# Performance work log

Hardware: AMD Instinct MI355X
Metric: run time of the kernel (lower is better)

The kernel has to match this reference:

```python
import jax, jax.numpy as jnp
import numpy as np

N_NODES = 20000
N_EDGES = 80000
D = 128       # in_dim_node == in_dim_edge == hidden dims
ITERS = 15    # mp_iterations
EPS = 1e-5    # torch LayerNorm default eps


def _mlp(h, W0, b0, W1, b1, W2, b2, gamma, beta):
    """Linear-ReLU-Linear-ReLU-Linear-LayerNorm (hidden_layers=2)."""
    h = jax.nn.relu(h @ W0 + b0)
    h = jax.nn.relu(h @ W1 + b1)
    h = h @ W2 + b2
    mu = jnp.mean(h, axis=-1, keepdims=True)
    var = jnp.var(h, axis=-1, keepdims=True)
    return gamma * (h - mu) * jax.lax.rsqrt(var + EPS) + beta


def setup_inputs() -> dict:
    key = jax.random.key(0)
    ks = iter(jax.random.split(key, 32))

    def lin(fi, fo):
        bnd = 1.0 / np.sqrt(fi)
        W = jax.random.uniform(next(ks), (ITERS, fi, fo), minval=-bnd, maxval=bnd, dtype=jnp.float32)
        b = jax.random.uniform(next(ks), (ITERS, fo), minval=-bnd, maxval=bnd, dtype=jnp.float32)
        return W, b

    x = jax.random.normal(next(ks), (N_NODES, D), dtype=jnp.float32)
    edge_attr = jax.random.normal(next(ks), (N_EDGES, D), dtype=jnp.float32)
    edge_index = jax.random.randint(next(ks), (2, N_EDGES), 0, N_NODES)

    eW0, eB0 = lin(3 * D, D)   # edge MLP input = cat(src, dest, edge) = 384
    eW1, eB1 = lin(D, D)
    eW2, eB2 = lin(D, D)
    nW0, nB0 = lin(2 * D, D)   # node MLP input = cat(x, agg) = 256
    nW1, nB1 = lin(D, D)
    nW2, nB2 = lin(D, D)
    ones = jnp.ones((ITERS, D), jnp.float32)
    zeros = jnp.zeros((ITERS, D), jnp.float32)

    return dict(x=x, edge_attr=edge_attr,
                eW0=eW0, eB0=eB0, eW1=eW1, eB1=eB1, eW2=eW2, eB2=eB2, eG=ones, eBeta=zeros,
                nW0=nW0, nB0=nB0, nW1=nW1, nB1=nB1, nW2=nW2, nB2=nB2, nG=ones, nBeta=zeros,
                edge_index=edge_index)


def reference(x, edge_attr, eW0, eB0, eW1, eB1, eW2, eB2, eG, eBeta,
              nW0, nB0, nW1, nB1, nW2, nB2, nG, nBeta, edge_index):
    row, col = edge_index[0], edge_index[1]
    n = x.shape[0]
    params = (eW0, eB0, eW1, eB1, eW2, eB2, eG, eBeta,
              nW0, nB0, nW1, nB1, nW2, nB2, nG, nBeta)

    def step(carry, p):
        xc, ec = carry
        (ew0, eb0, ew1, eb1, ew2, eb2, eg, ebt,
         nw0, nb0, nw1, nb1, nw2, nb2, ng, nbt) = p
        # EdgeProcessor: gather + MLP, then FullResidualConnection (add previous)
        e_in = jnp.concatenate([xc[row], xc[col], ec], axis=-1)        # [E, 3D]
        ec = _mlp(e_in, ew0, eb0, ew1, eb1, ew2, eb2, eg, ebt) + ec
        # NodeProcessor: scatter_sum over destination nodes + MLP + residual
        agg = jax.ops.segment_sum(ec, col, num_segments=n)             # [N, D]
        n_in = jnp.concatenate([xc, agg], axis=-1)                     # [N, 2D]
        xc = _mlp(n_in, nw0, nb0, nw1, nb1, nw2, nb2, ng, nbt) + xc
        return (xc, ec), None

    (x, edge_attr), _ = jax.lax.scan(step, (x, edge_attr), params)
    return x, edge_attr
```

## Files before the change

kernel.cpp:

```cpp
#include <hip/hip_runtime.h>
#include <hip/hip_bf16.h>

typedef __hip_bfloat16 bf16;
typedef __attribute__((ext_vector_type(8))) short short8;
typedef __attribute__((ext_vector_type(4))) float f32x4;

#define NN 20000
#define NE 80000
#define DD 128
#define NITER 15
#define HSTRIDE 136

__device__ inline void gload16(const void* g, void* l) {
  __builtin_amdgcn_global_load_lds(
      (const __attribute__((address_space(1))) void*)g,
      (__attribute__((address_space(3))) void*)l, 16, 0, 0);
}

__device__ inline void waitVm(int n) {
  switch (n) {
    case 0: asm volatile("s_waitcnt vmcnt(0)" ::: "memory"); break;
    case 1: asm volatile("s_waitcnt vmcnt(1)" ::: "memory"); break;
    case 2: asm volatile("s_waitcnt vmcnt(2)" ::: "memory"); break;
    case 3: asm volatile("s_waitcnt vmcnt(3)" ::: "memory"); break;
    default: asm volatile("s_waitcnt vmcnt(4)" ::: "memory"); break;
  }
}

__device__ inline float bfbits2f(unsigned int hi16) {
  union { unsigned int u; float f; } c; c.u = hi16; return c.f;
}

__device__ inline float readin(const void* p, int i, int fl) {
  return fl ? (float)((const bf16*)p)[i] : ((const float*)p)[i];
}

__global__ void detzero_kernel(const unsigned short* __restrict__ x,
                               int* __restrict__ counts, int* __restrict__ flag) {
  const int bid = blockIdx.x, t = threadIdx.x;
  if (bid < 79) {
    int i = bid * 256 + t;
    if (i < NN) counts[i] = 0;
    return;
  }
  __shared__ int cs[256], ct[256];
  int sane = 0, tot = 0;
  for (int i = 2 * t; i < 16384; i += 512) {
    unsigned short v = x[i];
    int e = (v >> 7) & 0xFF;
    tot++;
    if (v == 0 || (e >= 80 && e <= 170)) sane++;
  }
  cs[t] = sane; ct[t] = tot;
  __syncthreads();
  for (int o = 128; o > 0; o >>= 1) {
    if (t < o) { cs[t] += cs[t + o]; ct[t] += ct[t + o]; }
    __syncthreads();
  }
  if (t == 0) *flag = (cs[0] * 10 > ct[0] * 7) ? 1 : 0;
}

#define CX  (NN * DD)
#define CE  (NE * DD)
#define CW0 (NITER * 384 * DD)
#define CW1 (NITER * 128 * DD)
#define CNW0 (NITER * 256 * DD)
#define CB  (NITER * DD)
#define BX0 CX
#define BX1 (BX0 + CE)
#define BX7 (BX1 + CW0 + CW1 + CW1 + CNW0 + CW1 + CW1)
#define BX8 (BX7 + 10 * CB)

struct CvtP {
  const void *x, *e;
  const void* w[6];
  bf16 *xb, *eb;
  bf16* wt[6];
  const void* bs[10];
  float* bd[10];
  const int* flag;
};

__global__ void convert_all(CvtP P) {
  const int fl = *P.flag;
  const int gstride = gridDim.x * 256;
  for (int i = blockIdx.x * 256 + threadIdx.x; i < BX8; i += gstride) {
    if (i < BX0) {
      P.xb[i] = (bf16)readin(P.x, i, fl);
    } else if (i < BX1) {
      P.eb[i - BX0] = (bf16)readin(P.e, i - BX0, fl);
    } else if (i < BX7) {
      int j = i - BX1, w;
      if (j < CW0) { w = 0; }
      else if ((j -= CW0) < CW1) { w = 1; }
      else if ((j -= CW1) < CW1) { w = 2; }
      else if ((j -= CW1) < CNW0) { w = 3; }
      else if ((j -= CNW0) < CW1) { w = 4; }
      else { j -= CW1; w = 5; }
      const int K = (w == 0) ? 384 : (w == 3) ? 256 : 128;
      float v = readin(P.w[w], j, fl);
      int it = j / (K * DD);
      int rem = j - it * K * DD;
      int k = rem >> 7, n = rem & 127;
      P.wt[w][(size_t)it * K * DD + (size_t)n * K + k] = (bf16)v;
    } else {
      int j = i - BX7;
      int b = j / CB, r = j - b * CB;
      P.bd[b][r] = readin(P.bs[b], r, fl);
    }
  }
}

template<int K0, int AMODE, int NW>
__global__ __launch_bounds__(NW * 64, NW == 8 ? 6 : 4) void fused_mlp(
    const bf16* S0b,
    const bf16* S1b,
    const int*  __restrict__ eidx,
    const bf16* __restrict__ W0t, const bf16* __restrict__ W1t,
    const bf16* __restrict__ W2t,
    const float* __restrict__ b0, const float* __restrict__ b1,
    const float* __restrict__ b2,
    const float* __restrict__ gamma, const float* __restrict__ beta,
    bf16* st, int M)
{
  constexpr int NS1  = K0 / 32;
  constexpr int ROWS = NW * 16;
  constexpr int DN   = (NW == 8) ? 1 : 2;
  __shared__ __align__(16) bf16 Bls[2][128 * 32];
  __shared__ __align__(16) bf16 Hls[ROWS * HSTRIDE];

  const int tid  = threadIdx.x;
  const int lane = tid & 63;
  const int wv   = tid >> 6;
  const int l15  = lane & 15, quad = lane >> 4;
  const int m0   = blockIdx.x * ROWS;
  const int scol = tid >> 2;
  const int sk8  = (tid & 3) * 8;

  const int rowm = min(m0 + wv * 16 + l15, M - 1);
  int ir = 0, ic = 0;
  if (AMODE == 1) { ir = eidx[rowm]; ic = eidx[NE + rowm]; }

  auto dmaW = [&](const bf16* W, int K, int kk, int buf) {
    gload16(W + (size_t)scol * K + kk + sk8, &Bls[buf][scol * 32 + sk8]);
    if (NW == 4)
      gload16(W + (size_t)(scol + 64) * K + kk + sk8, &Bls[buf][(scol + 64) * 32 + sk8]);
  };
  auto gatherA = [&](int kk, short8* a) {
    const int ks = (kk & 127) + quad * 8;
    const bf16* base;
    if (AMODE == 1) {
      const int seg = kk >> 7;
      base = (seg == 0) ? S0b + (size_t)ir * DD
           : (seg == 1) ? S0b + (size_t)ic * DD
                        : S1b + (size_t)rowm * DD;
    } else {
      base = (kk >> 7) ? S1b + (size_t)rowm * DD
                       : S0b + (size_t)rowm * DD;
    }
    *a = *(const short8*)(base + ks);
  };

  f32x4 acc[8];
  auto zacc = [&]() {
#pragma unroll
    for (int j = 0; j < 8; j++) acc[j] = (f32x4){0.f, 0.f, 0.f, 0.f};
  };
  auto slabMfmaA = [&](short8 a, int buf) {
    short8 bfr[8];
#pragma unroll
    for (int ni = 0; ni < 8; ni++)
      bfr[ni] = *(const short8*)&Bls[buf][(ni * 16 + l15) * 32 + quad * 8];
#pragma unroll
    for (int ni = 0; ni < 8; ni++)
      acc[ni] = __builtin_amdgcn_mfma_f32_16x16x32_bf16(a, bfr[ni], acc[ni], 0, 0, 0);
  };
  auto slabMfmaH = [&](int kk, int buf) {
    short8 a = *(const short8*)&Hls[(wv * 16 + l15) * HSTRIDE + kk + quad * 8];
    short8 bfr[8];
#pragma unroll
    for (int ni = 0; ni < 8; ni++)
      bfr[ni] = *(const short8*)&Bls[buf][(ni * 16 + l15) * 32 + quad * 8];
#pragma unroll
    for (int ni = 0; ni < 8; ni++)
      acc[ni] = __builtin_amdgcn_mfma_f32_16x16x32_bf16(a, bfr[ni], acc[ni], 0, 0, 0);
  };
  auto writeH = [&](const float* bias) {
    float bv[8];
#pragma unroll
    for (int ni = 0; ni < 8; ni++) bv[ni] = bias[ni * 16 + l15];
#pragma unroll
    for (int r = 0; r < 4; r++) {
      const int row = wv * 16 + quad * 4 + r;
#pragma unroll
      for (int ni = 0; ni < 8; ni++)
        Hls[row * HSTRIDE + ni * 16 + l15] = (bf16)fmaxf(acc[ni][r] + bv[ni], 0.f);
    }
  };

  zacc();
  short8 aCur, aNxt;
  dmaW(W0t, K0, 0, 0);
  gatherA(0, &aCur);
#pragma unroll
  for (int s = 0; s < NS1; s++) {
    int cnt;
    if (s + 1 < NS1) {
      dmaW(W0t, K0, (s + 1) * 32, (s + 1) & 1);
      gatherA((s + 1) * 32, &aNxt);
      cnt = 1 + DN + 1;
    } else {
      dmaW(W1t, 128, 0, NS1 & 1);
      cnt = 1 + DN;
    }
    waitVm(cnt);
    __builtin_amdgcn_s_barrier();
    __builtin_amdgcn_sched_barrier(0);
    slabMfmaA(aCur, s & 1);
    __builtin_amdgcn_sched_barrier(0);
    __builtin_amdgcn_s_barrier();
    aCur = aNxt;
  }
  writeH(b0);

  zacc();
#pragma unroll
  for (int s = 0; s < 4; s++) {
    if (s < 3) dmaW(W1t, 128, (s + 1) * 32, (NS1 + s + 1) & 1);
    else       dmaW(W2t, 128, 0,            (NS1 + 4) & 1);
    waitVm(DN);
    __builtin_amdgcn_s_barrier();
    __builtin_amdgcn_sched_barrier(0);
    slabMfmaH(s * 32, (NS1 + s) & 1);
    __builtin_amdgcn_sched_barrier(0);
    __builtin_amdgcn_s_barrier();
  }
  writeH(b1);

  zacc();
#pragma unroll
  for (int s = 0; s < 4; s++) {
    int cnt = 0;
    if (s < 3) { dmaW(W2t, 128, (s + 1) * 32, (NS1 + 4 + s + 1) & 1); cnt = DN; }
    waitVm(cnt);
    __builtin_amdgcn_s_barrier();
    __builtin_amdgcn_sched_barrier(0);
    slabMfmaH(s * 32, (NS1 + 4 + s) & 1);
    if (s < 3) {
      __builtin_amdgcn_sched_barrier(0);
      __builtin_amdgcn_s_barrier();
    }
  }

  float bv[8], gv[8], btv[8];
#pragma unroll
  for (int ni = 0; ni < 8; ni++) {
    const int col = ni * 16 + l15;
    bv[ni] = b2[col]; gv[ni] = gamma[col]; btv[ni] = beta[col];
  }
#pragma unroll
  for (int r = 0; r < 4; r++) {
    float a = 0.f, bq = 0.f;
#pragma unroll
    for (int ni = 0; ni < 8; ni++) {
      const float v = acc[ni][r] + bv[ni];
      a += v; bq += v * v;
    }
#pragma unroll
    for (int off = 1; off < 16; off <<= 1) {
      a  += __shfl_xor(a, off);
      bq += __shfl_xor(bq, off);
    }
    const float mu = a * (1.0f / 128.0f);
    const float var = fmaxf(bq * (1.0f / 128.0f) - mu * mu, 0.0f);
    const float rs = rsqrtf(var + 1e-5f);
    const int m = m0 + wv * 16 + quad * 4 + r;
    if (m < M) {
#pragma unroll
      for (int ni = 0; ni < 8; ni++) {
        const int col = ni * 16 + l15;
        const float v = acc[ni][r] + bv[ni];
        const float lnv = (v - mu) * rs * gv[ni] + btv[ni];
        const size_t idx = (size_t)m * DD + col;
        st[idx] = (bf16)(lnv + (float)st[idx]);
      }
    }
  }
}

__global__ void hist_kernel(const int* __restrict__ eidx, int* __restrict__ counts) {
  int e = blockIdx.x * 256 + threadIdx.x;
  if (e < NE) atomicAdd(&counts[eidx[NE + e]], 1);
}

__global__ void scan_kernel(const int* __restrict__ counts, int* __restrict__ offs,
                            int* __restrict__ cursor) {
  __shared__ int sums[1024];
  const int t = threadIdx.x;
  const int base = t * 20;
  int local[20];
  int s = 0;
  for (int i = 0; i < 20; i++) {
    int idx = base + i;
    int c = (idx < NN) ? counts[idx] : 0;
    local[i] = s; s += c;
  }
  sums[t] = s;
  __syncthreads();
  for (int off = 1; off < 1024; off <<= 1) {
    int v = 0;
    if (t >= off) v = sums[t - off];
    __syncthreads();
    if (t >= off) sums[t] += v;
    __syncthreads();
  }
  int excl = (t == 0) ? 0 : sums[t - 1];
  for (int i = 0; i < 20; i++) {
    int idx = base + i;
    if (idx < NN) { offs[idx] = excl + local[i]; cursor[idx] = 0; }
  }
  if (t == 1023) offs[NN] = sums[1023];
}

__global__ void fill_kernel(const int* __restrict__ eidx, const int* __restrict__ offs,
                            int* __restrict__ cursor, int* __restrict__ sorted) {
  int e = blockIdx.x * 256 + threadIdx.x;
  if (e < NE) {
    int n = eidx[NE + e];
    int p = atomicAdd(&cursor[n], 1);
    sorted[offs[n] + p] = e;
  }
}

__global__ void aggregate_kernel(const bf16* __restrict__ eb, const int* __restrict__ offs,
                                 const int* __restrict__ sorted, bf16* __restrict__ aggb) {
  const int node = blockIdx.x * 4 + (threadIdx.x >> 6);
  const int lane = threadIdx.x & 63;
  if (node >= NN) return;
  const int s = offs[node], t = offs[node + 1];
  float a0 = 0.f, a1 = 0.f;
  for (int i = s; i < t; i++) {
    const int e = sorted[i];
    unsigned int v = *(const unsigned int*)(eb + (size_t)e * DD + 2 * lane);
    a0 += bfbits2f(v << 16);
    a1 += bfbits2f(v & 0xFFFF0000u);
  }
  bf16 o0 = (bf16)a0, o1 = (bf16)a1;
  unsigned int pack = (unsigned int)(*(unsigned short*)&o0)
                    | ((unsigned int)(*(unsigned short*)&o1) << 16);
  *(unsigned int*)(aggb + (size_t)node * DD + 2 * lane) = pack;
}

__global__ void outwb_kernel(const bf16* __restrict__ xb, const bf16* __restrict__ eb,
                             void* __restrict__ out, const int* __restrict__ flag) {
  int i = blockIdx.x * 256 + threadIdx.x;
  const int nx = NN * DD, total = (NN + NE) * DD;
  if (i < total) {
    bf16 v = (i < nx) ? xb[i] : eb[i - nx];
    if (*flag) ((bf16*)out)[i] = v;
    else       ((float*)out)[i] = (float)v;
  }
}

extern "C" void kernel_launch(void* const* d_in, const int* in_sizes, int n_in,
                              void* d_out, int out_size, void* d_ws, size_t ws_size,
                              hipStream_t stream) {
  const int* eidx = (const int*)d_in[18];

  char* ws = (char*)d_ws;
  size_t off = 0;
  auto alloc = [&](size_t bytes) -> char* {
    char* p = ws + off;
    off = (off + bytes + 255) & ~(size_t)255;
    return p;
  };

  bf16* xb   = (bf16*)alloc((size_t)NN * DD * 2);
  bf16* eb   = (bf16*)alloc((size_t)NE * DD * 2);
  bf16* aggb = (bf16*)alloc((size_t)NN * DD * 2);
  bf16* eW0t = (bf16*)alloc((size_t)CW0 * 2);
  bf16* eW1t = (bf16*)alloc((size_t)CW1 * 2);
  bf16* eW2t = (bf16*)alloc((size_t)CW1 * 2);
  bf16* nW0t = (bf16*)alloc((size_t)CNW0 * 2);
  bf16* nW1t = (bf16*)alloc((size_t)CW1 * 2);
  bf16* nW2t = (bf16*)alloc((size_t)CW1 * 2);
  float* bf_[10];
  for (int i = 0; i < 10; i++) bf_[i] = (float*)alloc(CB * 4);
  int* counts = (int*)alloc((size_t)NN * 4);
  int* cursor = (int*)alloc((size_t)NN * 4);
  int* offs   = (int*)alloc((size_t)(NN + 1) * 4);
  int* sorted = (int*)alloc((size_t)NE * 4);
  int* flag   = (int*)alloc(4);

  detzero_kernel<<<80, 256, 0, stream>>>((const unsigned short*)d_in[0], counts, flag);

  CvtP C;
  C.x = d_in[0]; C.e = d_in[1];
  C.w[0] = d_in[2];  C.w[1] = d_in[4];  C.w[2] = d_in[6];
  C.w[3] = d_in[10]; C.w[4] = d_in[12]; C.w[5] = d_in[14];
  C.xb = xb; C.eb = eb;
  C.wt[0] = eW0t; C.wt[1] = eW1t; C.wt[2] = eW2t;
  C.wt[3] = nW0t; C.wt[4] = nW1t; C.wt[5] = nW2t;
  const int bsrc_idx[10] = {3, 5, 7, 8, 9, 11, 13, 15, 16, 17};
  for (int i = 0; i < 10; i++) { C.bs[i] = d_in[bsrc_idx[i]]; C.bd[i] = bf_[i]; }
  C.flag = flag;
  convert_all<<<2048, 256, 0, stream>>>(C);

  hist_kernel<<<(NE + 255) / 256, 256, 0, stream>>>(eidx, counts);
  scan_kernel<<<1, 1024, 0, stream>>>(counts, offs, cursor);
  fill_kernel<<<(NE + 255) / 256, 256, 0, stream>>>(eidx, offs, cursor, sorted);

  const int egrid = NE / 128;
  const int ngrid = (NN + 63) / 64;

  for (int t = 0; t < NITER; t++) {
    fused_mlp<384, 1, 8><<<egrid, 512, 0, stream>>>(
        xb, eb, eidx,
        eW0t + (size_t)t * 384 * DD, eW1t + (size_t)t * 128 * DD,
        eW2t + (size_t)t * 128 * DD,
        bf_[0] + t * DD, bf_[1] + t * DD, bf_[2] + t * DD,
        bf_[3] + t * DD, bf_[4] + t * DD, eb, NE);
    aggregate_kernel<<<(NN + 3) / 4, 256, 0, stream>>>(eb, offs, sorted, aggb);
    fused_mlp<256, 2, 4><<<ngrid, 256, 0, stream>>>(
        xb, aggb, nullptr,
        nW0t + (size_t)t * 256 * DD, nW1t + (size_t)t * 128 * DD,
        nW2t + (size_t)t * 128 * DD,
        bf_[5] + t * DD, bf_[6] + t * DD, bf_[7] + t * DD,
        bf_[8] + t * DD, bf_[9] + t * DD, xb, NN);
  }

  outwb_kernel<<<((NN + NE) * DD + 255) / 256, 256, 0, stream>>>(xb, eb, d_out, flag);
}
```

Before: 1.098 ms.

## Give each wave two M-tiles in edge MLP and swizzle weight LDS layout

The edge MLP kernel now uses 4 waves, each handling two 16-row tiles (MI=2), so every B fragment read from LDS feeds twice as many MFMAs, halving weight LDS reads per row. Weights are stored with an XOR swizzle on the k-chunk so the LDS B-fragment reads avoid bank conflicts. The cost is more accumulator registers (launch bounds drop to 3 blocks per CU) and more outstanding loads, which needs extended vmcnt wait cases.

```diff
diff --git a/kernel.cpp b/kernel.cpp
--- a/kernel.cpp
+++ b/kernel.cpp
@@ -23,7 +23,9 @@
     case 1: asm volatile("s_waitcnt vmcnt(1)" ::: "memory"); break;
     case 2: asm volatile("s_waitcnt vmcnt(2)" ::: "memory"); break;
     case 3: asm volatile("s_waitcnt vmcnt(3)" ::: "memory"); break;
-    default: asm volatile("s_waitcnt vmcnt(4)" ::: "memory"); break;
+    case 4: asm volatile("s_waitcnt vmcnt(4)" ::: "memory"); break;
+    case 5: asm volatile("s_waitcnt vmcnt(5)" ::: "memory"); break;
+    default: asm volatile("s_waitcnt vmcnt(6)" ::: "memory"); break;
   }
 }
 
@@ -102,7 +104,9 @@
       int it = j / (K * DD);
       int rem = j - it * K * DD;
       int k = rem >> 7, n = rem & 127;
-      P.wt[w][(size_t)it * K * DD + (size_t)n * K + k] = (bf16)v;
+      int q  = (k >> 3) & 3;
+      int kp = (k & ~24) | (((q ^ ((n >> 1) & 3)) & 3) << 3);
+      P.wt[w][(size_t)it * K * DD + (size_t)n * K + kp] = (bf16)v;
     } else {
       int j = i - BX7;
       int b = j / CB, r = j - b * CB;
@@ -111,8 +115,8 @@
   }
 }
 
-template<int K0, int AMODE, int NW>
-__global__ __launch_bounds__(NW * 64, NW == 8 ? 6 : 4) void fused_mlp(
+template<int K0, int AMODE, int NW, int MI>
+__global__ __launch_bounds__(NW * 64, MI == 2 ? 3 : 4) void fused_mlp(
     const bf16* S0b,
     const bf16* S1b,
     const int*  __restrict__ eidx,
@@ -124,8 +128,9 @@
     bf16* st, int M)
 {
   constexpr int NS1  = K0 / 32;
-  constexpr int ROWS = NW * 16;
-  constexpr int DN   = (NW == 8) ? 1 : 2;
+  constexpr int RPW  = 16 * MI;
+  constexpr int ROWS = NW * RPW;
+  constexpr int DN   = 2;
   __shared__ __align__(16) bf16 Bls[2][128 * 32];
   __shared__ __align__(16) bf16 Hls[ROWS * HSTRIDE];
 
@@ -137,81 +142,99 @@
   const int scol = tid >> 2;
   const int sk8  = (tid & 3) * 8;
 
-  const int rowm = min(m0 + wv * 16 + l15, M - 1);
-  int ir = 0, ic = 0;
-  if (AMODE == 1) { ir = eidx[rowm]; ic = eidx[NE + rowm]; }
+  int rowm[MI], ir[MI], ic[MI];
+#pragma unroll
+  for (int g = 0; g < MI; g++) {
+    rowm[g] = min(m0 + wv * RPW + g * 16 + l15, M - 1);
+    ir[g] = 0; ic[g] = 0;
+    if (AMODE == 1) { ir[g] = eidx[rowm[g]]; ic[g] = eidx[NE + rowm[g]]; }
+  }
 
   auto dmaW = [&](const bf16* W, int K, int kk, int buf) {
-    gload16(W + (size_t)scol * K + kk + sk8, &Bls[buf][scol * 32 + sk8]);
-    if (NW == 4)
-      gload16(W + (size_t)(scol + 64) * K + kk + sk8, &Bls[buf][(scol + 64) * 32 + sk8]);
-  };
-  auto gatherA = [&](int kk, short8* a) {
+    gload16(W + (size_t)scol * K + kk + sk8,        &Bls[buf][scol * 32 + sk8]);
+    gload16(W + (size_t)(scol + 64) * K + kk + sk8, &Bls[buf][(scol + 64) * 32 + sk8]);
+  };
+  auto gatherA = [&](int g, int kk, short8* a) {
     const int ks = (kk & 127) + quad * 8;
     const bf16* base;
     if (AMODE == 1) {
       const int seg = kk >> 7;
-      base = (seg == 0) ? S0b + (size_t)ir * DD
-           : (seg == 1) ? S0b + (size_t)ic * DD
-                        : S1b + (size_t)rowm * DD;
+      base = (seg == 0) ? S0b + (size_t)ir[g] * DD
+           : (seg == 1) ? S0b + (size_t)ic[g] * DD
+                        : S1b + (size_t)rowm[g] * DD;
     } else {
-      base = (kk >> 7) ? S1b + (size_t)rowm * DD
-                       : S0b + (size_t)rowm * DD;
+      base = (kk >> 7) ? S1b + (size_t)rowm[g] * DD
+                       : S0b + (size_t)rowm[g] * DD;
     }
     *a = *(const short8*)(base + ks);
   };
 
-  f32x4 acc[8];
+  auto readB = [&](int buf, short8* bfr) {
+#pragma unroll
+    for (int ni = 0; ni < 8; ni++) {
+      const int r = ni * 16 + l15;
+      bfr[ni] = *(const short8*)&Bls[buf][r * 32 + ((quad ^ ((r >> 1) & 3)) & 3) * 8];
+    }
+  };
+
+  f32x4 acc[MI][8];
   auto zacc = [&]() {
 #pragma unroll
-    for (int j = 0; j < 8; j++) acc[j] = (f32x4){0.f, 0.f, 0.f, 0.f};
-  };
-  auto slabMfmaA = [&](short8 a, int buf) {
+    for (int g = 0; g < MI; g++)
+#pragma unroll
+      for (int j = 0; j < 8; j++) acc[g][j] = (f32x4){0.f, 0.f, 0.f, 0.f};
+  };
+  auto slabMfmaA = [&](short8* a, int buf) {
     short8 bfr[8];
-#pragma unroll
-    for (int ni = 0; ni < 8; ni++)
-      bfr[ni] = *(const short8*)&Bls[buf][(ni * 16 + l15) * 32 + quad * 8];
-#pragma unroll
-    for (int ni = 0; ni < 8; ni++)
-      acc[ni] = __builtin_amdgcn_mfma_f32_16x16x32_bf16(a, bfr[ni], acc[ni], 0, 0, 0);
+    readB(buf, bfr);
+#pragma unroll
+    for (int g = 0; g < MI; g++)
+#pragma unroll
+      for (int ni = 0; ni < 8; ni++)
+        acc[g][ni] = __builtin_amdgcn_mfma_f32_16x16x32_bf16(a[g], bfr[ni], acc[g][ni], 0, 0, 0);
   };
   auto slabMfmaH = [&](int kk, int buf) {
-    short8 a = *(const short8*)&Hls[(wv * 16 + l15) * HSTRIDE + kk + quad * 8];
     short8 bfr[8];
-#pragma unroll
-    for (int ni = 0; ni < 8; ni++)
-      bfr[ni] = *(const short8*)&Bls[buf][(ni * 16 + l15) * 32 + quad * 8];
-#pragma unroll
-    for (int ni = 0; ni < 8; ni++)
-      acc[ni] = __builtin_amdgcn_mfma_f32_16x16x32_bf16(a, bfr[ni], acc[ni], 0, 0, 0);
+    readB(buf, bfr);
+#pragma unroll
+    for (int g = 0; g < MI; g++) {
+      short8 a = *(const short8*)&Hls[(wv * RPW + g * 16 + l15) * HSTRIDE + kk + quad * 8];
+#pragma unroll
+      for (int ni = 0; ni < 8; ni++)
+        acc[g][ni] = __builtin_amdgcn_mfma_f32_16x16x32_bf16(a, bfr[ni], acc[g][ni], 0, 0, 0);
+    }
   };
   auto writeH = [&](const float* bias) {
     float bv[8];
 #pragma unroll
     for (int ni = 0; ni < 8; ni++) bv[ni] = bias[ni * 16 + l15];
 #pragma unroll
-    for (int r = 0; r < 4; r++) {
-      const int row = wv * 16 + quad * 4 + r;
-#pragma unroll
-      for (int ni = 0; ni < 8; ni++)
-        Hls[row * HSTRIDE + ni * 16 + l15] = (bf16)fmaxf(acc[ni][r] + bv[ni], 0.f);
-    }
+    for (int g = 0; g < MI; g++)
+#pragma unroll
+      for (int r = 0; r < 4; r++) {
+        const int row = wv * RPW + g * 16 + quad * 4 + r;
+#pragma unroll
+        for (int ni = 0; ni < 8; ni++)
+          Hls[row * HSTRIDE + ni * 16 + l15] = (bf16)fmaxf(acc[g][ni][r] + bv[ni], 0.f);
+      }
   };
 
   zacc();
-  short8 aCur, aNxt;
+  short8 aCur[MI], aNxt[MI];
   dmaW(W0t, K0, 0, 0);
-  gatherA(0, &aCur);
+#pragma unroll
+  for (int g = 0; g < MI; g++) gatherA(g, 0, &aCur[g]);
 #pragma unroll
   for (int s = 0; s < NS1; s++) {
     int cnt;
     if (s + 1 < NS1) {
       dmaW(W0t, K0, (s + 1) * 32, (s + 1) & 1);
-      gatherA((s + 1) * 32, &aNxt);
-      cnt = 1 + DN + 1;
+#pragma unroll
+      for (int g = 0; g < MI; g++) gatherA(g, (s + 1) * 32, &aNxt[g]);
+      cnt = MI + DN + MI;
     } else {
       dmaW(W1t, 128, 0, NS1 & 1);
-      cnt = 1 + DN;
+      cnt = MI + DN;
     }
     waitVm(cnt);
     __builtin_amdgcn_s_barrier();
@@ -219,7 +242,8 @@
     slabMfmaA(aCur, s & 1);
     __builtin_amdgcn_sched_barrier(0);
     __builtin_amdgcn_s_barrier();
-    aCur = aNxt;
+#pragma unroll
+    for (int g = 0; g < MI; g++) aCur[g] = aNxt[g];
   }
   writeH(b0);
 
@@ -259,30 +283,33 @@
     bv[ni] = b2[col]; gv[ni] = gamma[col]; btv[ni] = beta[col];
   }
 #pragma unroll
-  for (int r = 0; r < 4; r++) {
-    float a = 0.f, bq = 0.f;
-#pragma unroll
-    for (int ni = 0; ni < 8; ni++) {
-      const float v = acc[ni][r] + bv[ni];
-      a += v; bq += v * v;
-    }
-#pragma unroll
-    for (int off = 1; off < 16; off <<= 1) {
-      a  += __shfl_xor(a, off);
-      bq += __shfl_xor(bq, off);
-    }
-    const float mu = a * (1.0f / 128.0f);
-    const float var = fmaxf(bq * (1.0f / 128.0f) - mu * mu, 0.0f);
-    const float rs = rsqrtf(var + 1e-5f);
-    const int m = m0 + wv * 16 + quad * 4 + r;
-    if (m < M) {
+  for (int g = 0; g < MI; g++) {
+#pragma unroll
+    for (int r = 0; r < 4; r++) {
+      float a = 0.f, bq = 0.f;
 #pragma unroll
       for (int ni = 0; ni < 8; ni++) {
-        const int col = ni * 16 + l15;
-        const float v = acc[ni][r] + bv[ni];
-        const float lnv = (v - mu) * rs * gv[ni] + btv[ni];
-        const size_t idx = (size_t)m * DD + col;
-        st[idx] = (bf16)(lnv + (float)st[idx]);
+        const float v = acc[g][ni][r] + bv[ni];
+        a += v; bq += v * v;
+      }
+#pragma unroll
+      for (int off = 1; off < 16; off <<= 1) {
+        a  += __shfl_xor(a, off);
+        bq += __shfl_xor(bq, off);
+      }
+      const float mu = a * (1.0f / 128.0f);
+      const float var = fmaxf(bq * (1.0f / 128.0f) - mu * mu, 0.0f);
+      const float rs = rsqrtf(var + 1e-5f);
+      const int m = m0 + wv * RPW + g * 16 + quad * 4 + r;
+      if (m < M) {
+#pragma unroll
+        for (int ni = 0; ni < 8; ni++) {
+          const int col = ni * 16 + l15;
+          const float v = acc[g][ni][r] + bv[ni];
+          const float lnv = (v - mu) * rs * gv[ni] + btv[ni];
+          const size_t idx = (size_t)m * DD + col;
+          st[idx] = (bf16)(lnv + (float)st[idx]);
+        }
       }
     }
   }
@@ -414,14 +441,14 @@
   const int ngrid = (NN + 63) / 64;
 
   for (int t = 0; t < NITER; t++) {
-    fused_mlp<384, 1, 8><<<egrid, 512, 0, stream>>>(
+    fused_mlp<384, 1, 4, 2><<<egrid, 256, 0, stream>>>(
         xb, eb, eidx,
         eW0t + (size_t)t * 384 * DD, eW1t + (size_t)t * 128 * DD,
         eW2t + (size_t)t * 128 * DD,
         bf_[0] + t * DD, bf_[1] + t * DD, bf_[2] + t * DD,
         bf_[3] + t * DD, bf_[4] + t * DD, eb, NE);
     aggregate_kernel<<<(NN + 3) / 4, 256, 0, stream>>>(eb, offs, sorted, aggb);
-    fused_mlp<256, 2, 4><<<ngrid, 256, 0, stream>>>(
+    fused_mlp<256, 2, 4, 1><<<ngrid, 256, 0, stream>>>(
         xb, aggb, nullptr,
         nW0t + (size_t)t * 256 * DD, nW1t + (size_t)t * 128 * DD,
         nW2t + (size_t)t * 128 * DD,
```

Result: no change. 1.079 ms (-1.7%).
